# Kernel optimization log

Measured on AMD Instinct MI355X. Metric: run time of the kernel, lower is better.

Reference implementation:

```python
import jax, jax.numpy as jnp
import numpy as np

B, L, D, H, NS = 8, 1024, 64, 16, 3
DH = D // H          # head dim = 4 (scale = sqrt(4) = 2, matching K_.size(-1)**0.5)
DFF = 4 * D          # 256
EPS = 1e-5


def _bn(x_bld, gamma, beta):
    # BatchNorm1d in training mode on (B, C, L): normalize per-channel over (B, L)
    mean = jnp.mean(x_bld, axis=(0, 1))          # [D]
    var = jnp.mean((x_bld - mean) ** 2, axis=(0, 1))  # biased variance, as torch uses
    return gamma * (x_bld - mean) / jnp.sqrt(var + EPS) + beta


def setup_inputs() -> dict:
    key = jax.random.key(0)
    ks = jax.random.split(key, 12)
    s = 0.05
    inp = {
        "x": jax.random.normal(ks[0], (B, L, D), dtype=jnp.float32),
        # W_embed: Conv1d(64,64,k=1) == linear over channels
        "W_embed": jax.random.normal(ks[1], (D, D), dtype=jnp.float32) * s,
        "b_embed": jnp.zeros((D,), dtype=jnp.float32),
        "g0": jnp.ones((D,), dtype=jnp.float32),
        "be0": jnp.zeros((D,), dtype=jnp.float32),
        # shared attention weights (reused every stack)
        "Wq": jax.random.normal(ks[2], (D, D), dtype=jnp.float32) * s,
        "bq": jnp.zeros((D,), dtype=jnp.float32),
        "Wk": jax.random.normal(ks[3], (D, D), dtype=jnp.float32) * s,
        "bk": jnp.zeros((D,), dtype=jnp.float32),
        "Wv": jax.random.normal(ks[4], (D, D), dtype=jnp.float32) * s,
        "bv": jnp.zeros((D,), dtype=jnp.float32),
        "g_attn": jnp.ones((D,), dtype=jnp.float32),
        "be_attn": jnp.zeros((D,), dtype=jnp.float32),
        # shared feedforward (1x1 convs == channel linears)
        "W1": jax.random.normal(ks[5], (DFF, D), dtype=jnp.float32) * s,
        "b1": jnp.zeros((DFF,), dtype=jnp.float32),
        "W2": jax.random.normal(ks[6], (D, DFF), dtype=jnp.float32) * s,
        "b2": jnp.zeros((D,), dtype=jnp.float32),
        "g_ff": jnp.ones((D,), dtype=jnp.float32),
        "be_ff": jnp.zeros((D,), dtype=jnp.float32),
    }
    return inp


def reference(x, W_embed, b_embed, g0, be0, Wq, bq, Wk, bk, Wv, bv,
              g_attn, be_attn, W1, b1, W2, b2, g_ff, be_ff):
    # input embedding (1x1 conv) + batchnorm
    enc = x @ W_embed.T + b_embed              # [B, L, D]
    enc = _bn(enc, g0, be0)

    for _ in range(NS):  # num_stacks, SAME weights each stack (as in source)
        # --- multi-head attention (ReLU-activated QKV projections) ---
        Q = jax.nn.relu(enc @ Wq.T + bq)        # [B, L, D]
        K = jax.nn.relu(enc @ Wk.T + bk)
        V = jax.nn.relu(enc @ Wv.T + bv)
        q = Q.reshape(B, L, H, DH)
        k = K.reshape(B, L, H, DH)
        v = V.reshape(B, L, H, DH)
        scores = jnp.einsum('blhd,bmhd->bhlm', q, k) / jnp.sqrt(jnp.float32(DH))
        A = jax.nn.softmax(scores, axis=-1)     # [B, H, L, L]
        o = jnp.einsum('bhlm,bmhd->blhd', A, v).reshape(B, L, D)
        o = o + enc                             # residual
        enc = _bn(o, g_attn, be_attn)

        # --- feedforward: conv1d(k=1) -> ReLU -> conv1d(k=1) -> ReLU, residual, BN ---
        h = jax.nn.relu(enc @ W1.T + b1)        # [B, L, 4D]
        h = jax.nn.relu(h @ W2.T + b2)          # [B, L, D]
        h = h + enc                             # residual
        enc = _bn(h, g_ff, be_ff)
    return enc
```

## Files before the change

kernel.cpp:

```cpp
#include <hip/hip_runtime.h>
#include <math.h>

static constexpr int B_ = 8, L_ = 1024, D_ = 64, H_ = 16, DH_ = 4, DFF_ = 256;
static constexpr int M_ = B_ * L_;
static constexpr float EPS_ = 1e-5f;
static constexpr float INV_N_ = 1.0f / (float)M_;
static constexpr int PSTR_ = 128;

typedef _Float16 half4_ __attribute__((ext_vector_type(4)));
typedef __fp16   fp16x2 __attribute__((ext_vector_type(2)));
typedef float    f32x4  __attribute__((ext_vector_type(4)));

__global__ __launch_bounds__(256) void prep_kernel(
    const float* __restrict__ we, const float* __restrict__ wq,
    const float* __restrict__ wk, const float* __restrict__ wv,
    const float* __restrict__ w1, const float* __restrict__ w2,
    _Float16* __restrict__ dst)
{
    int e = blockIdx.x * 256 + threadIdx.x;
    float v;
    if      (e <  4096) v = we[e];
    else if (e <  8192) v = wq[e - 4096];
    else if (e < 12288) v = wk[e - 8192];
    else if (e < 16384) v = wv[e - 12288];
    else if (e < 32768) v = w1[e - 16384];
    else                v = w2[e - 32768];
    dst[e] = (_Float16)v;
}

template<int KT, int AF16, int BN_A, int RELU, int RESID_BN, int STATS, int OUTF16>
__device__ __forceinline__ void linear_mfma(
    const float* __restrict__ Af, const _Float16* __restrict__ Ah,
    const _Float16* __restrict__ Wh,
    const float* __restrict__ bias, const float* __restrict__ resid,
    float* __restrict__ Cf, _Float16* __restrict__ Ch, float outScale,
    int N, int m0, int n0,
    const float* __restrict__ partsIn, int npb,
    const float* __restrict__ gg, const float* __restrict__ bb,
    float* __restrict__ outParts, int blkIdx)
{
    constexpr int CPR = KT / 4;
    __shared__ half4_ Alds[64][CPR + 1];
    __shared__ half4_ Wlds[64][CPR + 1];
    __shared__ float  raw[128];
    __shared__ float  bnsc[64], bnsh[64];
    __shared__ float  wstats[4][128];
    const int t = threadIdx.x;

    if (BN_A || RESID_BN) {
        if (t < 128) {
            const float* pr = partsIn + (size_t)t * PSTR_;
            float a = 0.f;
            for (int j = 0; j < npb; j += 4) {
                float4 v4 = *(const float4*)&pr[j];
                a += v4.x + v4.y + v4.z + v4.w;
            }
            raw[t] = a;
        }
        __syncthreads();
        if (t < 64) {
            float mean = raw[t] * INV_N_;
            float ex2  = raw[64 + t] * INV_N_;
            float rs   = rsqrtf(ex2 - mean * mean + EPS_);
            float s2   = gg[t] * rs;
            bnsc[t] = s2;
            bnsh[t] = bb[t] - mean * s2;
        }
        __syncthreads();
    }

    {
        constexpr int ITERS = (64 * CPR) / 256;
        #pragma unroll
        for (int i = 0; i < ITERS; ++i) {
            int l = i * 256 + t;
            int row = l / CPR, c4 = l % CPR;
            half4_ hv;
            if (AF16) {
                hv = *(const half4_*)&Ah[(size_t)(m0 + row) * KT + c4 * 4];
            } else {
                float4 av = *(const float4*)&Af[(size_t)(m0 + row) * KT + c4 * 4];
                if (BN_A) {
                    int c = c4 * 4;
                    av.x = fmaf(av.x, bnsc[c + 0], bnsh[c + 0]);
                    av.y = fmaf(av.y, bnsc[c + 1], bnsh[c + 1]);
                    av.z = fmaf(av.z, bnsc[c + 2], bnsh[c + 2]);
                    av.w = fmaf(av.w, bnsc[c + 3], bnsh[c + 3]);
                }
                hv = half4_{(_Float16)av.x, (_Float16)av.y,
                            (_Float16)av.z, (_Float16)av.w};
            }
            Alds[row][c4] = hv;
            Wlds[row][c4] = *(const half4_*)&Wh[(size_t)(n0 + row) * KT + c4 * 4];
        }
    }
    __syncthreads();

    const int lane = t & 63, w = t >> 6, g = lane >> 4, ml = lane & 15;

    f32x4 acc[4] = {};
    #pragma unroll
    for (int kci = 0; kci < KT / 16; ++kci) {
        half4_ af = Alds[w * 16 + ml][kci * 4 + g];
        #pragma unroll
        for (int nt = 0; nt < 4; ++nt) {
            half4_ wf = Wlds[nt * 16 + ml][kci * 4 + g];
            acc[nt] = __builtin_amdgcn_mfma_f32_16x16x16f16(wf, af, acc[nt], 0, 0, 0);
        }
    }

    const int m = m0 + w * 16 + ml;
    float sv[4][4], qv[4][4];
    #pragma unroll
    for (int nt = 0; nt < 4; ++nt) {
        const int cb = nt * 16 + 4 * g;
        const int nc = n0 + cb;
        float4 bv4 = *(const float4*)&bias[nc];
        float r0 = acc[nt][0] + bv4.x, r1 = acc[nt][1] + bv4.y;
        float r2 = acc[nt][2] + bv4.z, r3 = acc[nt][3] + bv4.w;
        if (RELU) {
            r0 = fmaxf(r0, 0.f); r1 = fmaxf(r1, 0.f);
            r2 = fmaxf(r2, 0.f); r3 = fmaxf(r3, 0.f);
        }
        if (RESID_BN) {
            float4 rv = *(const float4*)&resid[(size_t)m * N + nc];
            r0 += fmaf(rv.x, bnsc[cb + 0], bnsh[cb + 0]);
            r1 += fmaf(rv.y, bnsc[cb + 1], bnsh[cb + 1]);
            r2 += fmaf(rv.z, bnsc[cb + 2], bnsh[cb + 2]);
            r3 += fmaf(rv.w, bnsc[cb + 3], bnsh[cb + 3]);
        }
        if (OUTF16) {
            half4_ hs = { (_Float16)(r0 * outScale), (_Float16)(r1 * outScale),
                          (_Float16)(r2 * outScale), (_Float16)(r3 * outScale) };
            *(half4_*)&Ch[(size_t)m * N + nc] = hs;
        } else {
            float4 o4 = { r0, r1, r2, r3 };
            *(float4*)&Cf[(size_t)m * N + nc] = o4;
        }
        if (STATS) {
            sv[nt][0] = r0; sv[nt][1] = r1; sv[nt][2] = r2; sv[nt][3] = r3;
            qv[nt][0] = r0 * r0; qv[nt][1] = r1 * r1;
            qv[nt][2] = r2 * r2; qv[nt][3] = r3 * r3;
        }
    }

    if (STATS) {
        #pragma unroll
        for (int d = 1; d <= 8; d <<= 1)
            #pragma unroll
            for (int nt = 0; nt < 4; ++nt)
                #pragma unroll
                for (int r = 0; r < 4; ++r) {
                    sv[nt][r] += __shfl_xor(sv[nt][r], d);
                    qv[nt][r] += __shfl_xor(qv[nt][r], d);
                }
        if (ml == 0) {
            #pragma unroll
            for (int nt = 0; nt < 4; ++nt)
                #pragma unroll
                for (int r = 0; r < 4; ++r) {
                    int ch = nt * 16 + 4 * g + r;
                    wstats[w][ch]      = sv[nt][r];
                    wstats[w][64 + ch] = qv[nt][r];
                }
        }
        __syncthreads();
        if (t < 128) {
            float a = wstats[0][t] + wstats[1][t] + wstats[2][t] + wstats[3][t];
            outParts[(size_t)t * PSTR_ + blkIdx] = a;
        }
    }
}

__global__ __launch_bounds__(256) void embed_kernel(
    const float* __restrict__ x, const _Float16* __restrict__ wemh,
    const float* __restrict__ bias, float* __restrict__ C,
    float* __restrict__ outParts)
{
    linear_mfma<64, 0, 0, 0, 0, 1, 0>(x, nullptr, wemh, bias, nullptr,
                                      C, nullptr, 1.f, 64, blockIdx.x * 64, 0,
                                      nullptr, 0, nullptr, nullptr,
                                      outParts, blockIdx.x);
}

__global__ __launch_bounds__(256) void qkv_kernel(
    const float* __restrict__ tmpA,
    const _Float16* __restrict__ wqh, const float* __restrict__ bq,
    const _Float16* __restrict__ wkh, const float* __restrict__ bk,
    const _Float16* __restrict__ wvh, const float* __restrict__ bv,
    _Float16* __restrict__ qh, _Float16* __restrict__ kh, _Float16* __restrict__ vh,
    const float* __restrict__ partsIn,
    const float* __restrict__ g, const float* __restrict__ be)
{
    const _Float16* W; const float* bias; _Float16* C; float sc2;
    if (blockIdx.y == 0)      { W = wqh; bias = bq; C = qh; sc2 = 0.5f * 1.44269504088896340736f; }
    else if (blockIdx.y == 1) { W = wkh; bias = bk; C = kh; sc2 = 1.f; }
    else                      { W = wvh; bias = bv; C = vh; sc2 = 1.f; }
    linear_mfma<64, 0, 1, 1, 0, 0, 1>(tmpA, nullptr, W, bias, nullptr,
                                      nullptr, C, sc2, 64, blockIdx.x * 64, 0,
                                      partsIn, 128, g, be, nullptr, 0);
}

__global__ __launch_bounds__(256) void ff1_kernel(
    const float* __restrict__ tmpB, const _Float16* __restrict__ w1h,
    const float* __restrict__ b1, _Float16* __restrict__ h1,
    const float* __restrict__ partsB,
    const float* __restrict__ g, const float* __restrict__ be)
{
    linear_mfma<64, 0, 1, 1, 0, 0, 1>(tmpB, nullptr, w1h, b1, nullptr,
                                      nullptr, h1, 1.f, 256,
                                      blockIdx.x * 64, blockIdx.y * 64,
                                      partsB, 64, g, be, nullptr, 0);
}

__global__ __launch_bounds__(256) void ff2_kernel(
    const _Float16* __restrict__ h1, const _Float16* __restrict__ w2h,
    const float* __restrict__ b2, const float* __restrict__ tmpB,
    float* __restrict__ tmpA, const float* __restrict__ partsB,
    const float* __restrict__ g, const float* __restrict__ be,
    float* __restrict__ partsOut)
{
    linear_mfma<256, 1, 0, 1, 1, 1, 0>(nullptr, h1, w2h, b2, tmpB,
                                       tmpA, nullptr, 1.f, 64, blockIdx.x * 64, 0,
                                       partsB, 64, g, be, partsOut, blockIdx.x);
}

__global__ __launch_bounds__(256) void attn_kernel(
    const _Float16* __restrict__ q, const _Float16* __restrict__ k,
    const _Float16* __restrict__ v, const float* __restrict__ encRaw,
    float* __restrict__ out, const float* __restrict__ partsIn,
    const float* __restrict__ gPrev, const float* __restrict__ bPrev,
    float* __restrict__ partsOut)
{
    __shared__ uint2    klds[1024];
    __shared__ _Float16 vstage[4][1040];
    __shared__ uint2    vlds[1024];
    __shared__ float    raw8[8], rsc[4], rsh[4];
    __shared__ float    wred[4][8];

    const int bid = blockIdx.x;
    const int qc  = bid & 7;
    const int h   = (bid >> 3) & 15;
    const int b   = bid >> 7;
    const int t   = threadIdx.x;

    if (t < 8) {
        const int row = (t >> 2) * 64 + 4 * h + (t & 3);
        const float* pr = partsIn + (size_t)row * PSTR_;
        float a = 0.f;
        for (int j = 0; j < 128; j += 4) {
            float4 v4 = *(const float4*)&pr[j];
            a += v4.x + v4.y + v4.z + v4.w;
        }
        raw8[t] = a;
    }

    const size_t baseh = (size_t)b * (L_ * D_) + h * DH_;

    #pragma unroll
    for (int i = 0; i < 4; ++i) {
        int key = i * 256 + t;
        klds[key] = *(const uint2*)&k[baseh + (size_t)key * D_];
        half4_ vv = __builtin_bit_cast(half4_, *(const uint2*)&v[baseh + (size_t)key * D_]);
        vstage[0][key] = vv[0]; vstage[1][key] = vv[1];
        vstage[2][key] = vv[2]; vstage[3][key] = vv[3];
    }
    __syncthreads();

    if (t < 4) {
        float mean = raw8[t] * INV_N_;
        float ex2  = raw8[4 + t] * INV_N_;
        float rs   = rsqrtf(ex2 - mean * mean + EPS_);
        float s2   = gPrev[4 * h + t] * rs;
        rsc[t] = s2;
        rsh[t] = bPrev[4 * h + t] - mean * s2;
    }

    #pragma unroll
    for (int i = 0; i < 4; ++i) {
        int e = i * 256 + t;
        int d = e & 3, g2 = (e >> 2) & 3, c = e >> 4;
        int k0 = c * 16 + g2 * 4;
        half4_ hv = { vstage[d][k0 + 0], vstage[d][k0 + 1],
                      vstage[d][k0 + 2], vstage[d][k0 + 3] };
        vlds[e] = __builtin_bit_cast(uint2, hv);
    }
    __syncthreads();

    const int lane = t & 63;
    const int wv2  = t >> 6;
    const int ln16 = lane & 15;
    const int g16  = lane >> 4;
    const int q0   = qc * 128 + wv2 * 32;

    half4_ qf0 = { 0, 0, 0, 0 }, qf1 = { 0, 0, 0, 0 };
    if (lane < 16) {
        qf0 = __builtin_bit_cast(half4_,
              *(const uint2*)&q[(size_t)(b * L_ + q0 + ln16) * D_ + h * DH_]);
        qf1 = __builtin_bit_cast(half4_,
              *(const uint2*)&q[(size_t)(b * L_ + q0 + 16 + ln16) * D_ + h * DH_]);
    }

    const half4_ ones = { (_Float16)1.f, (_Float16)1.f, (_Float16)1.f, (_Float16)1.f };
    const f32x4  fz   = { 0.f, 0.f, 0.f, 0.f };
    f32x4 o0 = fz, o1 = fz;

    #pragma unroll 2
    for (int c = 0; c < 64; ++c) {
        half4_ ka = __builtin_bit_cast(half4_, klds[c * 16 + ln16]);
        half4_ va = __builtin_bit_cast(half4_, vlds[c * 16 + g16 * 4 + (ln16 & 3)]);
        if (ln16 == 4) va = ones;

        f32x4 s0 = __builtin_amdgcn_mfma_f32_16x16x16f16(ka, qf0, fz, 0, 0, 0);
        f32x4 s1 = __builtin_amdgcn_mfma_f32_16x16x16f16(ka, qf1, fz, 0, 0, 0);

        float e00 = __builtin_amdgcn_exp2f(s0[0]);
        float e01 = __builtin_amdgcn_exp2f(s0[1]);
        float e02 = __builtin_amdgcn_exp2f(s0[2]);
        float e03 = __builtin_amdgcn_exp2f(s0[3]);
        float e10 = __builtin_amdgcn_exp2f(s1[0]);
        float e11 = __builtin_amdgcn_exp2f(s1[1]);
        float e12 = __builtin_amdgcn_exp2f(s1[2]);
        float e13 = __builtin_amdgcn_exp2f(s1[3]);

        fp16x2 a0 = __builtin_amdgcn_cvt_pkrtz(e00, e01);
        fp16x2 b0 = __builtin_amdgcn_cvt_pkrtz(e02, e03);
        fp16x2 a1 = __builtin_amdgcn_cvt_pkrtz(e10, e11);
        fp16x2 b1 = __builtin_amdgcn_cvt_pkrtz(e12, e13);
        half4_ p0 = __builtin_bit_cast(half4_, __builtin_shufflevector(a0, b0, 0, 1, 2, 3));
        half4_ p1 = __builtin_bit_cast(half4_, __builtin_shufflevector(a1, b1, 0, 1, 2, 3));

        o0 = __builtin_amdgcn_mfma_f32_16x16x16f16(va, p0, o0, 0, 0, 0);
        o1 = __builtin_amdgcn_mfma_f32_16x16x16f16(va, p1, o1, 0, 0, 0);
    }

    float ls0 = __shfl(o0[0], 16 + ln16);
    float ls1 = __shfl(o1[0], 16 + ln16);

    float4 r0v = { 0.f, 0.f, 0.f, 0.f }, r1v = r0v;
    if (lane < 16) {
        {
            const size_t gi = (size_t)(b * L_ + q0 + ln16) * D_ + h * DH_;
            const float inv = 1.0f / ls0;
            const float4 e4 = *(const float4*)&encRaw[gi];
            r0v.x = fmaf(o0[0], inv, fmaf(e4.x, rsc[0], rsh[0]));
            r0v.y = fmaf(o0[1], inv, fmaf(e4.y, rsc[1], rsh[1]));
            r0v.z = fmaf(o0[2], inv, fmaf(e4.z, rsc[2], rsh[2]));
            r0v.w = fmaf(o0[3], inv, fmaf(e4.w, rsc[3], rsh[3]));
            *(float4*)&out[gi] = r0v;
        }
        {
            const size_t gi = (size_t)(b * L_ + q0 + 16 + ln16) * D_ + h * DH_;
            const float inv = 1.0f / ls1;
            const float4 e4 = *(const float4*)&encRaw[gi];
            r1v.x = fmaf(o1[0], inv, fmaf(e4.x, rsc[0], rsh[0]));
            r1v.y = fmaf(o1[1], inv, fmaf(e4.y, rsc[1], rsh[1]));
            r1v.z = fmaf(o1[2], inv, fmaf(e4.z, rsc[2], rsh[2]));
            r1v.w = fmaf(o1[3], inv, fmaf(e4.w, rsc[3], rsh[3]));
            *(float4*)&out[gi] = r1v;
        }
    }

    float s4[4] = { r0v.x + r1v.x, r0v.y + r1v.y, r0v.z + r1v.z, r0v.w + r1v.w };
    float q4[4] = { r0v.x*r0v.x + r1v.x*r1v.x, r0v.y*r0v.y + r1v.y*r1v.y,
                    r0v.z*r0v.z + r1v.z*r1v.z, r0v.w*r0v.w + r1v.w*r1v.w };
    #pragma unroll
    for (int d2 = 1; d2 <= 8; d2 <<= 1) {
        #pragma unroll
        for (int j = 0; j < 4; ++j) {
            s4[j] += __shfl_xor(s4[j], d2);
            q4[j] += __shfl_xor(q4[j], d2);
        }
    }
    if (lane == 0) {
        #pragma unroll
        for (int j = 0; j < 4; ++j) { wred[wv2][j] = s4[j]; wred[wv2][4 + j] = q4[j]; }
    }
    __syncthreads();
    if (t < 8) {
        float a = wred[0][t] + wred[1][t] + wred[2][t] + wred[3][t];
        const int row = (t >> 2) * 64 + 4 * h + (t & 3);
        partsOut[(size_t)row * PSTR_ + (b * 8 + qc)] = a;
    }
}

__global__ __launch_bounds__(256) void bn_apply_kernel(
    const float* __restrict__ x, const float* __restrict__ parts,
    const float* __restrict__ gamma, const float* __restrict__ beta,
    float* __restrict__ y)
{
    __shared__ float fstats[128];
    const int t = threadIdx.x;
    if (t < 128) {
        const float* pr = parts + (size_t)t * PSTR_;
        float a = 0.f;
        for (int j = 0; j < 128; j += 4) {
            float4 v4 = *(const float4*)&pr[j];
            a += v4.x + v4.y + v4.z + v4.w;
        }
        fstats[t] = a;
    }
    __syncthreads();

    const int idx = blockIdx.x * 256 + t;
    const int c = (idx & 15) << 2;
    float4 xv = ((const float4*)x)[idx];
    float4 sm = *(const float4*)&fstats[c];
    float4 sq = *(const float4*)&fstats[64 + c];
    float4 g  = *(const float4*)&gamma[c];
    float4 be = *(const float4*)&beta[c];

    float mean[4] = {sm.x * INV_N_, sm.y * INV_N_, sm.z * INV_N_, sm.w * INV_N_};
    float ex2[4]  = {sq.x * INV_N_, sq.y * INV_N_, sq.z * INV_N_, sq.w * INV_N_};
    float xa[4] = {xv.x, xv.y, xv.z, xv.w};
    float ga[4] = {g.x, g.y, g.z, g.w};
    float ba[4] = {be.x, be.y, be.z, be.w};
    float ya[4];
    #pragma unroll
    for (int i = 0; i < 4; ++i) {
        float var = ex2[i] - mean[i] * mean[i];
        float rs = rsqrtf(var + EPS_);
        ya[i] = ga[i] * (xa[i] - mean[i]) * rs + ba[i];
    }
    float4 r = {ya[0], ya[1], ya[2], ya[3]};
    ((float4*)y)[idx] = r;
}

extern "C" void kernel_launch(void* const* d_in, const int* in_sizes, int n_in,
                              void* d_out, int out_size, void* d_ws, size_t ws_size,
                              hipStream_t stream)
{
    const float* x       = (const float*)d_in[0];
    const float* W_embed = (const float*)d_in[1];
    const float* b_embed = (const float*)d_in[2];
    const float* g0      = (const float*)d_in[3];
    const float* be0     = (const float*)d_in[4];
    const float* Wq      = (const float*)d_in[5];
    const float* bq      = (const float*)d_in[6];
    const float* Wk      = (const float*)d_in[7];
    const float* bk      = (const float*)d_in[8];
    const float* Wv      = (const float*)d_in[9];
    const float* bv      = (const float*)d_in[10];
    const float* g_attn  = (const float*)d_in[11];
    const float* be_attn = (const float*)d_in[12];
    const float* W1      = (const float*)d_in[13];
    const float* b1      = (const float*)d_in[14];
    const float* W2      = (const float*)d_in[15];
    const float* b2      = (const float*)d_in[16];
    const float* g_ff    = (const float*)d_in[17];
    const float* be_ff   = (const float*)d_in[18];

    float* ws     = (float*)d_ws;
    float* tmpA   = ws;
    float* tmpB   = ws + 524288;
    float* partsA = ws + 1048576;
    float* partsB = ws + 1064960;
    _Float16* hb  = (_Float16*)(ws + 1081344);
    _Float16* qh  = hb;
    _Float16* kh  = hb + 524288;
    _Float16* vh  = hb + 1048576;
    _Float16* h1  = hb + 1572864;
    _Float16* wemh = hb + 3670016;
    _Float16* wqh  = wemh + 4096;
    _Float16* wkh  = wqh + 4096;
    _Float16* wvh  = wkh + 4096;
    _Float16* w1h  = wvh + 4096;
    _Float16* w2h  = w1h + 16384;
    float* out = (float*)d_out;

    const dim3 blk(256);

    prep_kernel<<<192, blk, 0, stream>>>(W_embed, Wq, Wk, Wv, W1, W2, wemh);
    embed_kernel<<<128, blk, 0, stream>>>(x, wemh, b_embed, tmpA, partsA);

    for (int s = 0; s < 3; ++s) {
        const float* gP  = (s == 0) ? g0  : g_ff;
        const float* beP = (s == 0) ? be0 : be_ff;
        qkv_kernel<<<dim3(128, 3), blk, 0, stream>>>(
            tmpA, wqh, bq, wkh, bk, wvh, bv, qh, kh, vh, partsA, gP, beP);
        attn_kernel<<<1024, blk, 0, stream>>>(
            qh, kh, vh, tmpA, tmpB, partsA, gP, beP, partsB);
        ff1_kernel<<<dim3(128, 4), blk, 0, stream>>>(
            tmpB, w1h, b1, h1, partsB, g_attn, be_attn);
        ff2_kernel<<<128, blk, 0, stream>>>(
            h1, w2h, b2, tmpB, tmpA, partsB, g_attn, be_attn, partsA);
    }
    bn_apply_kernel<<<512, blk, 0, stream>>>(tmpA, partsA, g_ff, be_ff, out);
}
```

Before: 180.0 us.

## Split attention key range across wave pairs and double attention grid

Result: slower. 201.0 us (+11.6%).

```diff
diff --git a/kernel.cpp b/kernel.cpp
--- a/kernel.cpp
+++ b/kernel.cpp
@@ -210,7 +210,7 @@
     linear_mfma<64, 0, 1, 1, 0, 0, 1>(tmpB, nullptr, w1h, b1, nullptr,
                                       nullptr, h1, 1.f, 256,
                                       blockIdx.x * 64, blockIdx.y * 64,
-                                      partsB, 64, g, be, nullptr, 0);
+                                      partsB, 128, g, be, nullptr, 0);
 }
 
 __global__ __launch_bounds__(256) void ff2_kernel(
@@ -222,7 +222,7 @@
 {
     linear_mfma<256, 1, 0, 1, 1, 1, 0>(nullptr, h1, w2h, b2, tmpB,
                                        tmpA, nullptr, 1.f, 64, blockIdx.x * 64, 0,
-                                       partsB, 64, g, be, partsOut, blockIdx.x);
+                                       partsB, 128, g, be, partsOut, blockIdx.x);
 }
 
 __global__ __launch_bounds__(256) void attn_kernel(
@@ -236,12 +236,12 @@
     __shared__ _Float16 vstage[4][1040];
     __shared__ uint2    vlds[1024];
     __shared__ float    raw8[8], rsc[4], rsh[4];
-    __shared__ float    wred[4][8];
+    __shared__ float    wred[2][8];
 
     const int bid = blockIdx.x;
-    const int qc  = bid & 7;
-    const int h   = (bid >> 3) & 15;
-    const int b   = bid >> 7;
+    const int qc  = bid & 15;
+    const int h   = (bid >> 4) & 15;
+    const int b   = bid >> 8;
     const int t   = threadIdx.x;
 
     if (t < 8) {
@@ -289,9 +289,11 @@
 
     const int lane = t & 63;
     const int wv2  = t >> 6;
+    const int tp   = wv2 & 1;
+    const int half = wv2 >> 1;
     const int ln16 = lane & 15;
     const int g16  = lane >> 4;
-    const int q0   = qc * 128 + wv2 * 32;
+    const int q0   = qc * 64 + tp * 32;
 
     half4_ qf0 = { 0, 0, 0, 0 }, qf1 = { 0, 0, 0, 0 };
     if (lane < 16) {
@@ -306,7 +308,8 @@
     f32x4 o0 = fz, o1 = fz;
 
     #pragma unroll 2
-    for (int c = 0; c < 64; ++c) {
+    for (int cc = 0; cc < 32; ++cc) {
+        const int c = half * 32 + cc;
         half4_ ka = __builtin_bit_cast(half4_, klds[c * 16 + ln16]);
         half4_ va = __builtin_bit_cast(half4_, vlds[c * 16 + g16 * 4 + (ln16 & 3)]);
         if (ln16 == 4) va = ones;
@@ -334,53 +337,75 @@
         o1 = __builtin_amdgcn_mfma_f32_16x16x16f16(va, p1, o1, 0, 0, 0);
     }
 
-    float ls0 = __shfl(o0[0], 16 + ln16);
-    float ls1 = __shfl(o1[0], 16 + ln16);
+    __syncthreads();
+    if (wv2 >= 2) {
+        const int base = ((wv2 - 2) * 64 + lane) * 4;
+        klds[base + 0] = __builtin_bit_cast(uint2, float2{o0[0], o0[1]});
+        klds[base + 1] = __builtin_bit_cast(uint2, float2{o0[2], o0[3]});
+        klds[base + 2] = __builtin_bit_cast(uint2, float2{o1[0], o1[1]});
+        klds[base + 3] = __builtin_bit_cast(uint2, float2{o1[2], o1[3]});
+    }
+    __syncthreads();
 
     float4 r0v = { 0.f, 0.f, 0.f, 0.f }, r1v = r0v;
-    if (lane < 16) {
-        {
-            const size_t gi = (size_t)(b * L_ + q0 + ln16) * D_ + h * DH_;
-            const float inv = 1.0f / ls0;
-            const float4 e4 = *(const float4*)&encRaw[gi];
-            r0v.x = fmaf(o0[0], inv, fmaf(e4.x, rsc[0], rsh[0]));
-            r0v.y = fmaf(o0[1], inv, fmaf(e4.y, rsc[1], rsh[1]));
-            r0v.z = fmaf(o0[2], inv, fmaf(e4.z, rsc[2], rsh[2]));
-            r0v.w = fmaf(o0[3], inv, fmaf(e4.w, rsc[3], rsh[3]));
-            *(float4*)&out[gi] = r0v;
-        }
-        {
-            const size_t gi = (size_t)(b * L_ + q0 + 16 + ln16) * D_ + h * DH_;
-            const float inv = 1.0f / ls1;
-            const float4 e4 = *(const float4*)&encRaw[gi];
-            r1v.x = fmaf(o1[0], inv, fmaf(e4.x, rsc[0], rsh[0]));
-            r1v.y = fmaf(o1[1], inv, fmaf(e4.y, rsc[1], rsh[1]));
-            r1v.z = fmaf(o1[2], inv, fmaf(e4.z, rsc[2], rsh[2]));
-            r1v.w = fmaf(o1[3], inv, fmaf(e4.w, rsc[3], rsh[3]));
-            *(float4*)&out[gi] = r1v;
-        }
-    }
-
-    float s4[4] = { r0v.x + r1v.x, r0v.y + r1v.y, r0v.z + r1v.z, r0v.w + r1v.w };
-    float q4[4] = { r0v.x*r0v.x + r1v.x*r1v.x, r0v.y*r0v.y + r1v.y*r1v.y,
-                    r0v.z*r0v.z + r1v.z*r1v.z, r0v.w*r0v.w + r1v.w*r1v.w };
-    #pragma unroll
-    for (int d2 = 1; d2 <= 8; d2 <<= 1) {
+    float s4[4] = {}, q4[4] = {};
+    if (wv2 < 2) {
+        const int base = (wv2 * 64 + lane) * 4;
+        float2 p0a = __builtin_bit_cast(float2, klds[base + 0]);
+        float2 p0b = __builtin_bit_cast(float2, klds[base + 1]);
+        float2 p1a = __builtin_bit_cast(float2, klds[base + 2]);
+        float2 p1b = __builtin_bit_cast(float2, klds[base + 3]);
+        o0[0] += p0a.x; o0[1] += p0a.y; o0[2] += p0b.x; o0[3] += p0b.y;
+        o1[0] += p1a.x; o1[1] += p1a.y; o1[2] += p1b.x; o1[3] += p1b.y;
+
+        float ls0 = __shfl(o0[0], 16 + ln16);
+        float ls1 = __shfl(o1[0], 16 + ln16);
+
+        if (lane < 16) {
+            {
+                const size_t gi = (size_t)(b * L_ + q0 + ln16) * D_ + h * DH_;
+                const float inv = 1.0f / ls0;
+                const float4 e4 = *(const float4*)&encRaw[gi];
+                r0v.x = fmaf(o0[0], inv, fmaf(e4.x, rsc[0], rsh[0]));
+                r0v.y = fmaf(o0[1], inv, fmaf(e4.y, rsc[1], rsh[1]));
+                r0v.z = fmaf(o0[2], inv, fmaf(e4.z, rsc[2], rsh[2]));
+                r0v.w = fmaf(o0[3], inv, fmaf(e4.w, rsc[3], rsh[3]));
+                *(float4*)&out[gi] = r0v;
+            }
+            {
+                const size_t gi = (size_t)(b * L_ + q0 + 16 + ln16) * D_ + h * DH_;
+                const float inv = 1.0f / ls1;
+                const float4 e4 = *(const float4*)&encRaw[gi];
+                r1v.x = fmaf(o1[0], inv, fmaf(e4.x, rsc[0], rsh[0]));
+                r1v.y = fmaf(o1[1], inv, fmaf(e4.y, rsc[1], rsh[1]));
+                r1v.z = fmaf(o1[2], inv, fmaf(e4.z, rsc[2], rsh[2]));
+                r1v.w = fmaf(o1[3], inv, fmaf(e4.w, rsc[3], rsh[3]));
+                *(float4*)&out[gi] = r1v;
+            }
+        }
+
+        s4[0] = r0v.x + r1v.x; s4[1] = r0v.y + r1v.y;
+        s4[2] = r0v.z + r1v.z; s4[3] = r0v.w + r1v.w;
+        q4[0] = r0v.x*r0v.x + r1v.x*r1v.x; q4[1] = r0v.y*r0v.y + r1v.y*r1v.y;
+        q4[2] = r0v.z*r0v.z + r1v.z*r1v.z; q4[3] = r0v.w*r0v.w + r1v.w*r1v.w;
         #pragma unroll
-        for (int j = 0; j < 4; ++j) {
-            s4[j] += __shfl_xor(s4[j], d2);
-            q4[j] += __shfl_xor(q4[j], d2);
-        }
-    }
-    if (lane == 0) {
-        #pragma unroll
-        for (int j = 0; j < 4; ++j) { wred[wv2][j] = s4[j]; wred[wv2][4 + j] = q4[j]; }
+        for (int d2 = 1; d2 <= 8; d2 <<= 1) {
+            #pragma unroll
+            for (int j = 0; j < 4; ++j) {
+                s4[j] += __shfl_xor(s4[j], d2);
+                q4[j] += __shfl_xor(q4[j], d2);
+            }
+        }
+        if (lane == 0) {
+            #pragma unroll
+            for (int j = 0; j < 4; ++j) { wred[wv2][j] = s4[j]; wred[wv2][4 + j] = q4[j]; }
+        }
     }
     __syncthreads();
     if (t < 8) {
-        float a = wred[0][t] + wred[1][t] + wred[2][t] + wred[3][t];
+        float a = wred[0][t] + wred[1][t];
         const int row = (t >> 2) * 64 + 4 * h + (t & 3);
-        partsOut[(size_t)row * PSTR_ + (b * 8 + qc)] = a;
+        partsOut[(size_t)row * PSTR_ + (b * 16 + qc)] = a;
     }
 }
 
@@ -478,7 +503,7 @@
         const float* beP = (s == 0) ? be0 : be_ff;
         qkv_kernel<<<dim3(128, 3), blk, 0, stream>>>(
             tmpA, wqh, bq, wkh, bk, wvh, bv, qh, kh, vh, partsA, gP, beP);
-        attn_kernel<<<1024, blk, 0, stream>>>(
+        attn_kernel<<<2048, blk, 0, stream>>>(
             qh, kh, vh, tmpA, tmpB, partsA, gP, beP, partsB);
         ff1_kernel<<<dim3(128, 4), blk, 0, stream>>>(
             tmpB, w1h, b1, h1, partsB, g_attn, be_attn);
```

## Write Q/K/V in head-major layouts from a dedicated QKV MFMA kernel

Applied to the files above, without the earlier changes.

Result: faster. 159.8 us (-11.2%).

```diff
diff --git a/kernel.cpp b/kernel.cpp
--- a/kernel.cpp
+++ b/kernel.cpp
@@ -190,15 +190,92 @@
     const _Float16* __restrict__ wvh, const float* __restrict__ bv,
     _Float16* __restrict__ qh, _Float16* __restrict__ kh, _Float16* __restrict__ vh,
     const float* __restrict__ partsIn,
-    const float* __restrict__ g, const float* __restrict__ be)
-{
-    const _Float16* W; const float* bias; _Float16* C; float sc2;
-    if (blockIdx.y == 0)      { W = wqh; bias = bq; C = qh; sc2 = 0.5f * 1.44269504088896340736f; }
-    else if (blockIdx.y == 1) { W = wkh; bias = bk; C = kh; sc2 = 1.f; }
-    else                      { W = wvh; bias = bv; C = vh; sc2 = 1.f; }
-    linear_mfma<64, 0, 1, 1, 0, 0, 1>(tmpA, nullptr, W, bias, nullptr,
-                                      nullptr, C, sc2, 64, blockIdx.x * 64, 0,
-                                      partsIn, 128, g, be, nullptr, 0);
+    const float* __restrict__ gg, const float* __restrict__ bb)
+{
+    __shared__ half4_ Alds[64][17];
+    __shared__ half4_ Wlds[64][17];
+    __shared__ float  raw[128];
+    __shared__ float  bnsc[64], bnsh[64];
+    const int t    = threadIdx.x;
+    const int m0   = blockIdx.x * 64;
+    const int mode = blockIdx.y;
+
+    const _Float16* W = (mode == 0) ? wqh : (mode == 1) ? wkh : wvh;
+    const float* bias = (mode == 0) ? bq  : (mode == 1) ? bk  : bv;
+    const float  sc2  = (mode == 0) ? 0.5f * 1.44269504088896340736f : 1.f;
+
+    if (t < 128) {
+        const float* pr = partsIn + (size_t)t * PSTR_;
+        float a = 0.f;
+        for (int j = 0; j < 128; j += 4) {
+            float4 v4 = *(const float4*)&pr[j];
+            a += v4.x + v4.y + v4.z + v4.w;
+        }
+        raw[t] = a;
+    }
+    __syncthreads();
+    if (t < 64) {
+        float mean = raw[t] * INV_N_;
+        float ex2  = raw[64 + t] * INV_N_;
+        float rs   = rsqrtf(ex2 - mean * mean + EPS_);
+        float s2   = gg[t] * rs;
+        bnsc[t] = s2;
+        bnsh[t] = bb[t] - mean * s2;
+    }
+    __syncthreads();
+
+    #pragma unroll
+    for (int i = 0; i < 4; ++i) {
+        int l = i * 256 + t;
+        int row = l >> 4, c4 = l & 15;
+        float4 av = *(const float4*)&tmpA[(size_t)(m0 + row) * 64 + c4 * 4];
+        int c = c4 * 4;
+        av.x = fmaf(av.x, bnsc[c + 0], bnsh[c + 0]);
+        av.y = fmaf(av.y, bnsc[c + 1], bnsh[c + 1]);
+        av.z = fmaf(av.z, bnsc[c + 2], bnsh[c + 2]);
+        av.w = fmaf(av.w, bnsc[c + 3], bnsh[c + 3]);
+        Alds[row][c4] = half4_{(_Float16)av.x, (_Float16)av.y,
+                               (_Float16)av.z, (_Float16)av.w};
+        Wlds[row][c4] = *(const half4_*)&W[(size_t)row * 64 + c4 * 4];
+    }
+    __syncthreads();
+
+    const int lane = t & 63, w = t >> 6, g = lane >> 4, ml = lane & 15;
+
+    f32x4 acc[4] = {};
+    #pragma unroll
+    for (int kci = 0; kci < 4; ++kci) {
+        half4_ af = Alds[w * 16 + ml][kci * 4 + g];
+        #pragma unroll
+        for (int nt = 0; nt < 4; ++nt) {
+            half4_ wf = Wlds[nt * 16 + ml][kci * 4 + g];
+            acc[nt] = __builtin_amdgcn_mfma_f32_16x16x16f16(wf, af, acc[nt], 0, 0, 0);
+        }
+    }
+
+    const int m    = m0 + w * 16 + ml;
+    const int bidx = m >> 10, row = m & 1023;
+    #pragma unroll
+    for (int nt = 0; nt < 4; ++nt) {
+        const int nc = nt * 16 + 4 * g;
+        const int h  = nc >> 2;
+        float4 bv4 = *(const float4*)&bias[nc];
+        float r0 = fmaxf(acc[nt][0] + bv4.x, 0.f) * sc2;
+        float r1 = fmaxf(acc[nt][1] + bv4.y, 0.f) * sc2;
+        float r2 = fmaxf(acc[nt][2] + bv4.z, 0.f) * sc2;
+        float r3 = fmaxf(acc[nt][3] + bv4.w, 0.f) * sc2;
+        if (mode == 2) {
+            size_t base = ((size_t)(bidx * 16 + h) * 4) * 1024 + row;
+            vh[base + 0]    = (_Float16)r0;
+            vh[base + 1024] = (_Float16)r1;
+            vh[base + 2048] = (_Float16)r2;
+            vh[base + 3072] = (_Float16)r3;
+        } else {
+            _Float16* C = (mode == 0) ? qh : kh;
+            half4_ hs = { (_Float16)r0, (_Float16)r1, (_Float16)r2, (_Float16)r3 };
+            *(half4_*)&C[((size_t)(bidx * 16 + h) * 1024 + row) * 4] = hs;
+        }
+    }
 }
 
 __global__ __launch_bounds__(256) void ff1_kernel(
@@ -232,11 +309,10 @@
     const float* __restrict__ gPrev, const float* __restrict__ bPrev,
     float* __restrict__ partsOut)
 {
-    __shared__ uint2    klds[1024];
-    __shared__ _Float16 vstage[4][1040];
-    __shared__ uint2    vlds[1024];
-    __shared__ float    raw8[8], rsc[4], rsh[4];
-    __shared__ float    wred[4][8];
+    __shared__ uint2 klds[1024];
+    __shared__ uint2 vlds[1024];
+    __shared__ float raw8[8], rsc[4], rsh[4];
+    __shared__ float wred[4][8];
 
     const int bid = blockIdx.x;
     const int qc  = bid & 7;
@@ -254,19 +330,6 @@
         }
         raw8[t] = a;
     }
-
-    const size_t baseh = (size_t)b * (L_ * D_) + h * DH_;
-
-    #pragma unroll
-    for (int i = 0; i < 4; ++i) {
-        int key = i * 256 + t;
-        klds[key] = *(const uint2*)&k[baseh + (size_t)key * D_];
-        half4_ vv = __builtin_bit_cast(half4_, *(const uint2*)&v[baseh + (size_t)key * D_]);
-        vstage[0][key] = vv[0]; vstage[1][key] = vv[1];
-        vstage[2][key] = vv[2]; vstage[3][key] = vv[3];
-    }
-    __syncthreads();
-
     if (t < 4) {
         float mean = raw8[t] * INV_N_;
         float ex2  = raw8[4 + t] * INV_N_;
@@ -276,14 +339,14 @@
         rsh[t] = bPrev[4 * h + t] - mean * s2;
     }
 
+    const size_t baseqk = (size_t)(b * 16 + h) * 4096;
+
     #pragma unroll
     for (int i = 0; i < 4; ++i) {
-        int e = i * 256 + t;
-        int d = e & 3, g2 = (e >> 2) & 3, c = e >> 4;
-        int k0 = c * 16 + g2 * 4;
-        half4_ hv = { vstage[d][k0 + 0], vstage[d][k0 + 1],
-                      vstage[d][k0 + 2], vstage[d][k0 + 3] };
-        vlds[e] = __builtin_bit_cast(uint2, hv);
+        int key = i * 256 + t;
+        klds[key] = *(const uint2*)&k[baseqk + (size_t)key * 4];
+        int e = (t >> 2) * 16 + (t & 3) * 4 + i;
+        vlds[e] = *(const uint2*)&v[baseqk + (size_t)i * 1024 + t * 4];
     }
     __syncthreads();
 
@@ -296,16 +359,16 @@
     half4_ qf0 = { 0, 0, 0, 0 }, qf1 = { 0, 0, 0, 0 };
     if (lane < 16) {
         qf0 = __builtin_bit_cast(half4_,
-              *(const uint2*)&q[(size_t)(b * L_ + q0 + ln16) * D_ + h * DH_]);
+              *(const uint2*)&q[baseqk + (size_t)(q0 + ln16) * 4]);
         qf1 = __builtin_bit_cast(half4_,
-              *(const uint2*)&q[(size_t)(b * L_ + q0 + 16 + ln16) * D_ + h * DH_]);
+              *(const uint2*)&q[baseqk + (size_t)(q0 + 16 + ln16) * 4]);
     }
 
     const half4_ ones = { (_Float16)1.f, (_Float16)1.f, (_Float16)1.f, (_Float16)1.f };
     const f32x4  fz   = { 0.f, 0.f, 0.f, 0.f };
     f32x4 o0 = fz, o1 = fz;
 
-    #pragma unroll 2
+    #pragma unroll 4
     for (int c = 0; c < 64; ++c) {
         half4_ ka = __builtin_bit_cast(half4_, klds[c * 16 + ln16]);
         half4_ va = __builtin_bit_cast(half4_, vlds[c * 16 + g16 * 4 + (ln16 & 3)]);
```
